# Kernel optimization log

Hardware: AMD Instinct MI355X
Metric: run time of the kernel (lower is better)

Reference implementation:

```python
import jax, jax.numpy as jnp
import numpy as np

DIM = 128
HEADS = 4
K = 7          # neighborhood kernel size
MLP_RATIO = 4
EPS = 1e-5


def setup_inputs() -> dict:
    key = jax.random.key(0)
    ks = jax.random.split(key, 8)
    B, H, W, C = 4, 64, 64, DIM
    hid = C * MLP_RATIO
    s = lambda k, shape: jax.random.normal(k, shape, jnp.float32) * 0.02
    return {
        "x": jax.random.normal(ks[0], (B, H, W, C), jnp.float32),
        "ln1_g": jnp.ones((C,), jnp.float32),
        "ln1_b": jnp.zeros((C,), jnp.float32),
        "qkv_w": s(ks[1], (C, 3 * C)),
        "qkv_b": jnp.zeros((3 * C,), jnp.float32),
        "rpb": s(ks[2], (HEADS, 2 * K - 1, 2 * K - 1)),
        "proj_w": s(ks[3], (C, C)),
        "proj_b": jnp.zeros((C,), jnp.float32),
        "ln2_g": jnp.ones((C,), jnp.float32),
        "ln2_b": jnp.zeros((C,), jnp.float32),
        "fc1_w": s(ks[4], (C, hid)),
        "fc1_b": jnp.zeros((hid,), jnp.float32),
        "fc2_w": s(ks[5], (hid, C)),
        "fc2_b": jnp.zeros((C,), jnp.float32),
    }


def _ln(x, g, b):
    m = jnp.mean(x, axis=-1, keepdims=True)
    v = jnp.mean(jnp.square(x - m), axis=-1, keepdims=True)
    return (x - m) * jax.lax.rsqrt(v + EPS) * g + b


def _neigh_idx(L, k):
    # NATTEN border-clamped neighborhood: start = clamp(i - k//2, 0, L-k)
    i = jnp.arange(L)
    start = jnp.clip(i - k // 2, 0, L - k)
    idx = start[:, None] + jnp.arange(k)[None, :]        # [L, k] key positions
    rel = idx - i[:, None] + (k - 1)                     # [L, k] rpb indices in [0, 2k-2]
    return idx, rel


def _neighborhood_attention(x, qkv_w, qkv_b, rpb, proj_w, proj_b):
    B, H, W, C = x.shape
    nh, hd = HEADS, C // HEADS
    scale = hd ** -0.5
    qkv = (x @ qkv_w + qkv_b).reshape(B, H, W, 3, nh, hd)
    qkv = qkv.transpose(3, 0, 4, 1, 2, 5)                # [3, B, nh, H, W, hd]
    q, k_, v = qkv[0] * scale, qkv[1], qkv[2]
    ih, rh = _neigh_idx(H, K)
    iw, rw = _neigh_idx(W, K)
    # gather 7x7 neighborhoods: [B, nh, H, K, W, K, hd]
    kg = k_[:, :, ih][:, :, :, :, iw]
    vg = v[:, :, ih][:, :, :, :, iw]
    attn = jnp.einsum('bnywc,bnykxjc->bnyxkj', q, kg)    # [B, nh, H, W, K, K]
    bias = rpb[:, rh][:, :, :, rw]                       # [nh, H, K, W, K]
    attn = attn + bias.transpose(0, 1, 3, 2, 4)[None]
    a = jax.nn.softmax(attn.reshape(B, nh, H, W, K * K), axis=-1)
    a = a.reshape(B, nh, H, W, K, K)
    out = jnp.einsum('bnyxkj,bnykxjc->bnyxc', a, vg)     # [B, nh, H, W, hd]
    out = out.transpose(0, 2, 3, 1, 4).reshape(B, H, W, C)
    return out @ proj_w + proj_b


def reference(x, ln1_g, ln1_b, qkv_w, qkv_b, rpb, proj_w, proj_b,
              ln2_g, ln2_b, fc1_w, fc1_b, fc2_w, fc2_b):
    h = x + _neighborhood_attention(_ln(x, ln1_g, ln1_b), qkv_w, qkv_b, rpb, proj_w, proj_b)
    y = _ln(h, ln2_g, ln2_b)
    y = jax.nn.gelu(y @ fc1_w + fc1_b, approximate=False) @ fc2_w + fc2_b
    return h + y
```

## Files before the change

kernel.cpp:

```cpp
#include <hip/hip_runtime.h>
#include <math.h>

#define TOKS 16384
#define CDIM 128
#define NH 4
#define HD 32
#define HID 512
#define QSCALE 0.17677669529663687f
#define LEPS 1e-5f

typedef const float* fp;
typedef const unsigned short* bfp16;
typedef __attribute__((ext_vector_type(8))) short bf16x8;
typedef __attribute__((ext_vector_type(4))) float f32x4;

__device__ inline unsigned int bfp2(float a, float b) {
    unsigned int ua = __float_as_uint(a); ua = (ua + 0x7FFFu + ((ua >> 16) & 1u)) >> 16;
    unsigned int ub = __float_as_uint(b); ub = (ub + 0x7FFFu + ((ub >> 16) & 1u)) >> 16;
    return ua | (ub << 16);
}
__device__ inline unsigned short bf1(float a) {
    unsigned int u = __float_as_uint(a);
    return (unsigned short)((u + 0x7FFFu + ((u >> 16) & 1u)) >> 16);
}
__device__ inline float lo16(unsigned int u) { return __uint_as_float(u << 16); }
__device__ inline float hi16(unsigned int u) { return __uint_as_float(u & 0xFFFF0000u); }

__global__ __launch_bounds__(256) void prep(fp qw, fp pw, fp f1w, fp f2w,
                                            fp x, fp g, fp b,
                                            unsigned short* __restrict__ wt,
                                            unsigned short* __restrict__ xn) {
    const int bid = blockIdx.x;
    if (bid < 768) {
        int e = bid * 256 + threadIdx.x;
        float v;
        if (e < 49152)       { int n = e >> 7,  k = e & 127;          v = qw[(size_t)k * 384 + n]; }
        else if (e < 65536)  { int i = e - 49152;  int n = i >> 7, k = i & 127; v = pw[(size_t)k * 128 + n]; }
        else if (e < 131072) { int i = e - 65536;  int n = i >> 7, k = i & 127; v = f1w[(size_t)k * 512 + n]; }
        else                 { int i = e - 131072; int n = i >> 9, k = i & 511; v = f2w[(size_t)k * 128 + n]; }
        wt[e] = bf1(v);
    } else {
        const int t = threadIdx.x;
        const int row = (bid - 768) * 8 + (t >> 5);
        const int l = t & 31;
        const float4 v = *(const float4*)(x + (size_t)row * CDIM + l * 4);
        float s = v.x + v.y + v.z + v.w;
        float q = v.x * v.x + v.y * v.y + v.z * v.z + v.w * v.w;
#pragma unroll
        for (int m = 16; m >= 1; m >>= 1) { s += __shfl_xor(s, m); q += __shfl_xor(q, m); }
        float mu = s * (1.f / 128.f);
        float rs = rsqrtf(q * (1.f / 128.f) - mu * mu + LEPS);
        const float4 gv = *(const float4*)(g + l * 4);
        const float4 bv = *(const float4*)(b + l * 4);
        float a0 = (v.x - mu) * rs * gv.x + bv.x, a1 = (v.y - mu) * rs * gv.y + bv.y;
        float a2 = (v.z - mu) * rs * gv.z + bv.z, a3 = (v.w - mu) * rs * gv.w + bv.w;
        uint2 o; o.x = bfp2(a0, a1); o.y = bfp2(a2, a3);
        *(uint2*)(xn + (size_t)row * CDIM + l * 4) = o;
    }
}


__global__ __launch_bounds__(256) void k1_mfma(bfp16 xn, bfp16 wt0, fp wb,
                                               float* __restrict__ qb,
                                               unsigned short* __restrict__ kvb) {
    __shared__ unsigned int lds[12288];
    const int m0 = blockIdx.x * 128;
    const int nb = blockIdx.y * 64;
    const int tid = threadIdx.x;
#pragma unroll
    for (int i = 0; i < 8; i++) {
        int slot = tid + i * 256;
        int m = slot >> 4, c16 = slot & 15;
        const uint4 v4 = *(const uint4*)(xn + (size_t)(m0 + m) * CDIM + c16 * 8);
        *(uint4*)&lds[m * 64 + (c16 ^ (m & 15)) * 4] = v4;
    }
#pragma unroll
    for (int i = 0; i < 4; i++) {
        int slot = tid + i * 256;
        int n = slot >> 4, c16 = slot & 15;
        const uint4 v4 = *(const uint4*)(wt0 + (size_t)(nb + n) * 128 + c16 * 8);
        *(uint4*)&lds[8192 + n * 64 + (c16 ^ (n & 15)) * 4] = v4;
    }
    __syncthreads();

    const int lane = tid & 63, wid = tid >> 6, quad = lane >> 4, l16 = lane & 15;
    f32x4 acc[2][4];
#pragma unroll
    for (int mt = 0; mt < 2; mt++)
#pragma unroll
        for (int nt = 0; nt < 4; nt++) acc[mt][nt] = (f32x4){0.f, 0.f, 0.f, 0.f};
#pragma unroll
    for (int kk = 0; kk < 4; kk++) {
        int c = kk * 4 + quad;
        bf16x8 a0 = *(bf16x8*)&lds[(wid * 32 + l16) * 64 + (c ^ l16) * 4];
        bf16x8 a1 = *(bf16x8*)&lds[(wid * 32 + 16 + l16) * 64 + (c ^ l16) * 4];
#pragma unroll
        for (int nt = 0; nt < 4; nt++) {
            bf16x8 bf = *(bf16x8*)&lds[8192 + (nt * 16 + l16) * 64 + (c ^ l16) * 4];
            acc[0][nt] = __builtin_amdgcn_mfma_f32_16x16x32_bf16(a0, bf, acc[0][nt], 0, 0, 0);
            acc[1][nt] = __builtin_amdgcn_mfma_f32_16x16x32_bf16(a1, bf, acc[1][nt], 0, 0, 0);
        }
    }
#pragma unroll
    for (int nt = 0; nt < 4; nt++) {
        int col = nb + nt * 16 + l16;
        float bias = wb[col];
#pragma unroll
        for (int mt = 0; mt < 2; mt++)
#pragma unroll
            for (int r = 0; r < 4; r++) {
                int row = m0 + wid * 32 + mt * 16 + quad * 4 + r;
                float vres = acc[mt][nt][r] + bias;
                if (col < 128)
                    qb[(size_t)row * 128 + col] = vres * QSCALE;
                else if (col < 256)
                    kvb[(size_t)row * 256 + (col - 128)] = bf1(vres);
                else
                    kvb[(size_t)row * 256 + 128 + (col - 256)] = bf1(vres);
            }
    }
}

__global__ __launch_bounds__(256) void k2_attn(const float* __restrict__ qb,
                                               const unsigned short* __restrict__ kvb,
                                               fp rpb, unsigned short* __restrict__ attnb) {
    const int gid = blockIdx.x * 256 + threadIdx.x;
    const int d = gid & 3;
    const int g = (gid >> 2) & 3;
    const int head = (gid >> 4) & 3;
    const int token = gid >> 6;
    const int bb = token >> 12;
    const int y = (token >> 6) & 63;
    const int xx = token & 63;
    const int sy = min(max(y - 3, 0), 57);
    const int sx = min(max(xx - 3, 0), 57);

    const int koff = head * HD + d * 8;
    float q[8];
    {
        const float4* qp = (const float4*)(qb + (size_t)token * 128 + koff);
        float4 q0 = qp[0], q1 = qp[1];
        q[0] = q0.x; q[1] = q0.y; q[2] = q0.z; q[3] = q0.w;
        q[4] = q1.x; q[5] = q1.y; q[6] = q1.z; q[7] = q1.w;
    }

    const float* rp = rpb + head * 169 + (sy - y + 6) * 13 + (sx - xx + 6);
    const int nbase = (bb << 12) + sy * 64 + sx;

    float sc[13];
#pragma unroll
    for (int i = 0; i < 13; i++) {
        int n = g * 13 + i;
        bool ok = n < 49;
        int nn = ok ? n : 48;
        int dy = nn / 7, dx = nn - dy * 7;
        const uint4 kk = *(const uint4*)(kvb + (size_t)(nbase + dy * 64 + dx) * 256 + koff);
        float s = q[0] * lo16(kk.x) + q[1] * hi16(kk.x)
                + q[2] * lo16(kk.y) + q[3] * hi16(kk.y)
                + q[4] * lo16(kk.z) + q[5] * hi16(kk.z)
                + q[6] * lo16(kk.w) + q[7] * hi16(kk.w);
        s += __shfl_xor(s, 1);
        s += __shfl_xor(s, 2);
        sc[i] = ok ? (s + rp[dy * 13 + dx]) : -1e30f;
    }
    float mx = sc[0];
#pragma unroll
    for (int l = 1; l < 13; l++) mx = fmaxf(mx, sc[l]);
    mx = fmaxf(mx, __shfl_xor(mx, 4));
    mx = fmaxf(mx, __shfl_xor(mx, 8));
    float sum = 0.f;
#pragma unroll
    for (int l = 0; l < 13; l++) { sc[l] = __expf(sc[l] - mx); sum += sc[l]; }
    sum += __shfl_xor(sum, 4);
    sum += __shfl_xor(sum, 8);
    float inv = 1.f / sum;

    float o[8];
#pragma unroll
    for (int i = 0; i < 8; i++) o[i] = 0.f;
#pragma unroll
    for (int i = 0; i < 13; i++) {
        int n = g * 13 + i;
        int nn = (n < 49) ? n : 48;
        int dy = nn / 7, dx = nn - dy * 7;
        float p = sc[i] * inv;
        const uint4 vv = *(const uint4*)(kvb + (size_t)(nbase + dy * 64 + dx) * 256 + 128 + koff);
        o[0] += p * lo16(vv.x); o[1] += p * hi16(vv.x);
        o[2] += p * lo16(vv.y); o[3] += p * hi16(vv.y);
        o[4] += p * lo16(vv.z); o[5] += p * hi16(vv.z);
        o[6] += p * lo16(vv.w); o[7] += p * hi16(vv.w);
    }
#pragma unroll
    for (int i = 0; i < 8; i++) {
        o[i] += __shfl_xor(o[i], 4);
        o[i] += __shfl_xor(o[i], 8);
    }
    if (g == 0) {
        uint4 ov;
        ov.x = bfp2(o[0], o[1]); ov.y = bfp2(o[2], o[3]);
        ov.z = bfp2(o[4], o[5]); ov.w = bfp2(o[6], o[7]);
        *(uint4*)(attnb + (size_t)token * 128 + koff) = ov;
    }
}

__global__ __launch_bounds__(256) void k3_mfma(bfp16 attnb, fp x, bfp16 wt1, fp pb,
                                               fp g2, fp b2,
                                               float* __restrict__ h,
                                               unsigned short* __restrict__ hn) {
    __shared__ unsigned int lds[12288];
    const int m0 = blockIdx.x * 64;
    const int tid = threadIdx.x;
#pragma unroll
    for (int i = 0; i < 4; i++) {
        int slot = tid + i * 256;
        int m = slot >> 4, c16 = slot & 15;
        const uint4 v4 = *(const uint4*)(attnb + (size_t)(m0 + m) * CDIM + c16 * 8);
        *(uint4*)&lds[m * 64 + (c16 ^ (m & 15)) * 4] = v4;
    }
#pragma unroll
    for (int i = 0; i < 8; i++) {
        int slot = tid + i * 256;
        int n = slot >> 4, c16 = slot & 15;
        const uint4 v4 = *(const uint4*)(wt1 + (size_t)n * 128 + c16 * 8);
        *(uint4*)&lds[4096 + n * 64 + (c16 ^ (n & 15)) * 4] = v4;
    }
    __syncthreads();

    const int lane = tid & 63, wid = tid >> 6, quad = lane >> 4, l16 = lane & 15;
    const int mrow = wid * 16 + l16;
    f32x4 acc[8];
#pragma unroll
    for (int nt = 0; nt < 8; nt++) acc[nt] = (f32x4){0.f, 0.f, 0.f, 0.f};
#pragma unroll
    for (int kk = 0; kk < 4; kk++) {
        int c = kk * 4 + quad;
        bf16x8 a = *(bf16x8*)&lds[mrow * 64 + (c ^ l16) * 4];
#pragma unroll
        for (int nt = 0; nt < 8; nt++) {
            bf16x8 bf = *(bf16x8*)&lds[4096 + (nt * 16 + l16) * 64 + (c ^ l16) * 4];
            acc[nt] = __builtin_amdgcn_mfma_f32_16x16x32_bf16(a, bf, acc[nt], 0, 0, 0);
        }
    }
    float s[4] = {0.f, 0.f, 0.f, 0.f}, q[4] = {0.f, 0.f, 0.f, 0.f};
#pragma unroll
    for (int nt = 0; nt < 8; nt++) {
        int col = nt * 16 + l16;
        float bias = pb[col];
#pragma unroll
        for (int r = 0; r < 4; r++) {
            int row = m0 + wid * 16 + quad * 4 + r;
            float hv = x[(size_t)row * CDIM + col] + acc[nt][r] + bias;
            h[(size_t)row * CDIM + col] = hv;
            acc[nt][r] = hv;
            s[r] += hv; q[r] += hv * hv;
        }
    }
#pragma unroll
    for (int m = 1; m <= 8; m <<= 1) {
#pragma unroll
        for (int r = 0; r < 4; r++) {
            s[r] += __shfl_xor(s[r], m);
            q[r] += __shfl_xor(q[r], m);
        }
    }
    float mu[4], rs[4];
#pragma unroll
    for (int r = 0; r < 4; r++) {
        mu[r] = s[r] * (1.f / 128.f);
        rs[r] = rsqrtf(q[r] * (1.f / 128.f) - mu[r] * mu[r] + LEPS);
    }
#pragma unroll
    for (int nt = 0; nt < 8; nt++) {
        int col = nt * 16 + l16;
        float gg = g2[col], bb = b2[col];
#pragma unroll
        for (int r = 0; r < 4; r++) {
            int row = m0 + wid * 16 + quad * 4 + r;
            hn[(size_t)row * CDIM + col] = bf1((acc[nt][r] - mu[r]) * rs[r] * gg + bb);
        }
    }
}

__global__ __launch_bounds__(256) void k4_mfma(bfp16 hn, bfp16 wt2, fp wb,
                                               unsigned short* __restrict__ y1) {
    __shared__ unsigned int lds[12288];
    const int m0 = blockIdx.x * 128;
    const int nb = blockIdx.y * 64;
    const int tid = threadIdx.x;
#pragma unroll
    for (int i = 0; i < 8; i++) {
        int slot = tid + i * 256;
        int m = slot >> 4, c16 = slot & 15;
        const uint4 v4 = *(const uint4*)(hn + (size_t)(m0 + m) * CDIM + c16 * 8);
        *(uint4*)&lds[m * 64 + (c16 ^ (m & 15)) * 4] = v4;
    }
#pragma unroll
    for (int i = 0; i < 4; i++) {
        int slot = tid + i * 256;
        int n = slot >> 4, c16 = slot & 15;
        const uint4 v4 = *(const uint4*)(wt2 + (size_t)(nb + n) * 128 + c16 * 8);
        *(uint4*)&lds[8192 + n * 64 + (c16 ^ (n & 15)) * 4] = v4;
    }
    __syncthreads();

    const int lane = tid & 63, wid = tid >> 6, quad = lane >> 4, l16 = lane & 15;
    f32x4 acc[2][4];
#pragma unroll
    for (int mt = 0; mt < 2; mt++)
#pragma unroll
        for (int nt = 0; nt < 4; nt++) acc[mt][nt] = (f32x4){0.f, 0.f, 0.f, 0.f};
#pragma unroll
    for (int kk = 0; kk < 4; kk++) {
        int c = kk * 4 + quad;
        bf16x8 a0 = *(bf16x8*)&lds[(wid * 32 + l16) * 64 + (c ^ l16) * 4];
        bf16x8 a1 = *(bf16x8*)&lds[(wid * 32 + 16 + l16) * 64 + (c ^ l16) * 4];
#pragma unroll
        for (int nt = 0; nt < 4; nt++) {
            bf16x8 bf = *(bf16x8*)&lds[8192 + (nt * 16 + l16) * 64 + (c ^ l16) * 4];
            acc[0][nt] = __builtin_amdgcn_mfma_f32_16x16x32_bf16(a0, bf, acc[0][nt], 0, 0, 0);
            acc[1][nt] = __builtin_amdgcn_mfma_f32_16x16x32_bf16(a1, bf, acc[1][nt], 0, 0, 0);
        }
    }
#pragma unroll
    for (int nt = 0; nt < 4; nt++) {
        int col = nb + nt * 16 + l16;
        float bias = wb[col];
#pragma unroll
        for (int mt = 0; mt < 2; mt++)
#pragma unroll
            for (int r = 0; r < 4; r++) {
                int row = m0 + wid * 32 + mt * 16 + quad * 4 + r;
                float z = acc[mt][nt][r] + bias;
                y1[(size_t)row * HID + col] = bf1(0.5f * z * (1.f + erff(z * 0.70710678118654752f)));
            }
    }
}

__global__ __launch_bounds__(256) void k5_mfma(bfp16 y1, fp h, bfp16 wt3, fp wb,
                                               float* __restrict__ out) {
    __shared__ unsigned int lds[12288];
    const int m0 = blockIdx.x * 128;
    const int nb = blockIdx.y * 64;
    const int tid = threadIdx.x;
    const int lane = tid & 63, wid = tid >> 6, quad = lane >> 4, l16 = lane & 15;
    f32x4 acc[2][4];
#pragma unroll
    for (int mt = 0; mt < 2; mt++)
#pragma unroll
        for (int nt = 0; nt < 4; nt++) acc[mt][nt] = (f32x4){0.f, 0.f, 0.f, 0.f};

    for (int kc = 0; kc < 4; kc++) {
        if (kc) __syncthreads();
#pragma unroll
        for (int i = 0; i < 8; i++) {
            int slot = tid + i * 256;
            int m = slot >> 4, c16 = slot & 15;
            const uint4 v4 = *(const uint4*)(y1 + (size_t)(m0 + m) * HID + kc * 128 + c16 * 8);
            *(uint4*)&lds[m * 64 + (c16 ^ (m & 15)) * 4] = v4;
        }
#pragma unroll
        for (int i = 0; i < 4; i++) {
            int slot = tid + i * 256;
            int n = slot >> 4, c16 = slot & 15;
            const uint4 v4 = *(const uint4*)(wt3 + (size_t)(nb + n) * 512 + kc * 128 + c16 * 8);
            *(uint4*)&lds[8192 + n * 64 + (c16 ^ (n & 15)) * 4] = v4;
        }
        __syncthreads();
#pragma unroll
        for (int kk = 0; kk < 4; kk++) {
            int c = kk * 4 + quad;
            bf16x8 a0 = *(bf16x8*)&lds[(wid * 32 + l16) * 64 + (c ^ l16) * 4];
            bf16x8 a1 = *(bf16x8*)&lds[(wid * 32 + 16 + l16) * 64 + (c ^ l16) * 4];
#pragma unroll
            for (int nt = 0; nt < 4; nt++) {
                bf16x8 bf = *(bf16x8*)&lds[8192 + (nt * 16 + l16) * 64 + (c ^ l16) * 4];
                acc[0][nt] = __builtin_amdgcn_mfma_f32_16x16x32_bf16(a0, bf, acc[0][nt], 0, 0, 0);
                acc[1][nt] = __builtin_amdgcn_mfma_f32_16x16x32_bf16(a1, bf, acc[1][nt], 0, 0, 0);
            }
        }
    }
#pragma unroll
    for (int nt = 0; nt < 4; nt++) {
        int col = nb + nt * 16 + l16;
        float bias = wb[col];
#pragma unroll
        for (int mt = 0; mt < 2; mt++)
#pragma unroll
            for (int r = 0; r < 4; r++) {
                int row = m0 + wid * 32 + mt * 16 + quad * 4 + r;
                out[(size_t)row * CDIM + col] = h[(size_t)row * CDIM + col] + acc[mt][nt][r] + bias;
            }
    }
}

extern "C" void kernel_launch(void* const* d_in, const int* in_sizes, int n_in,
                              void* d_out, int out_size, void* d_ws, size_t ws_size,
                              hipStream_t stream) {
    fp x      = (fp)d_in[0];
    fp ln1_g  = (fp)d_in[1];
    fp ln1_b  = (fp)d_in[2];
    fp qkv_w  = (fp)d_in[3];
    fp qkv_b  = (fp)d_in[4];
    fp rpb    = (fp)d_in[5];
    fp proj_w = (fp)d_in[6];
    fp proj_b = (fp)d_in[7];
    fp ln2_g  = (fp)d_in[8];
    fp ln2_b  = (fp)d_in[9];
    fp fc1_w  = (fp)d_in[10];
    fp fc1_b  = (fp)d_in[11];
    fp fc2_w  = (fp)d_in[12];
    fp fc2_b  = (fp)d_in[13];
    float* out = (float*)d_out;

    float* ws = (float*)d_ws;
    float* h  = ws;
    unsigned short* xn = (unsigned short*)(h + (size_t)TOKS * CDIM);
    unsigned short* hn = xn + (size_t)TOKS * CDIM;
    float* qb = (float*)(hn + (size_t)TOKS * CDIM);
    unsigned short* kvb   = (unsigned short*)(qb + (size_t)TOKS * CDIM);
    unsigned short* attnb = kvb + (size_t)TOKS * 256;
    unsigned short* wt    = attnb + (size_t)TOKS * CDIM;
    unsigned short* y1    = (unsigned short*)qb;

    unsigned short* wt0 = wt;
    unsigned short* wt1 = wt + 49152;
    unsigned short* wt2 = wt + 65536;
    unsigned short* wt3 = wt + 131072;

    prep<<<768 + TOKS / 8, 256, 0, stream>>>(qkv_w, proj_w, fc1_w, fc2_w, x, ln1_g, ln1_b, wt, xn);
    k1_mfma<<<dim3(TOKS / 128, 6), 256, 0, stream>>>(xn, wt0, qkv_b, qb, kvb);
    k2_attn<<<TOKS * NH * 16 / 256, 256, 0, stream>>>(qb, kvb, rpb, attnb);
    k3_mfma<<<TOKS / 64, 256, 0, stream>>>(attnb, x, wt1, proj_b, ln2_g, ln2_b, h, hn);
    k4_mfma<<<dim3(TOKS / 128, 8), 256, 0, stream>>>(hn, wt2, fc1_b, y1);
    k5_mfma<<<dim3(TOKS / 128, 2), 256, 0, stream>>>(y1, h, wt3, fc2_b, out);
}
```

Before: 149.3 us.

## Stage K/V neighborhood halo in LDS for 2x2 query tiles in attention kernel

```diff
diff --git a/kernel.cpp b/kernel.cpp
--- a/kernel.cpp
+++ b/kernel.cpp
@@ -124,28 +124,42 @@
 __global__ __launch_bounds__(256) void k2_attn(const float* __restrict__ qb,
                                                const unsigned short* __restrict__ kvb,
                                                fp rpb, unsigned short* __restrict__ attnb) {
-    const int gid = blockIdx.x * 256 + threadIdx.x;
-    const int d = gid & 3;
-    const int g = (gid >> 2) & 3;
-    const int head = (gid >> 4) & 3;
-    const int token = gid >> 6;
-    const int bb = token >> 12;
-    const int y = (token >> 6) & 63;
-    const int xx = token & 63;
-    const int sy = min(max(y - 3, 0), 57);
-    const int sx = min(max(xx - 3, 0), 57);
-
-    const int koff = head * HD + d * 8;
+    __shared__ unsigned int ldsu[64 * 68];
+    const int tile = blockIdx.x;
+    const int bb = blockIdx.y;
+    const int ty0 = (tile >> 5) * 2, tx0 = (tile & 31) * 2;
+    const int ky0 = min(max(ty0 - 3, 0), 56);
+    const int kx0 = min(max(tx0 - 3, 0), 56);
+    const int tid = threadIdx.x;
+
+#pragma unroll
+    for (int i = 0; i < 4; i++) {
+        int slot = tid + i * 256;
+        int p = slot >> 4, c16 = slot & 15;
+        int gr = (bb << 12) + (ky0 + (p >> 3)) * 64 + kx0 + (p & 7);
+        const uint4 v4 = *(const uint4*)(kvb + (size_t)gr * 256 + c16 * 8);
+        *(uint4*)&ldsu[p * 68 + c16 * 4] = v4;
+    }
+
+    const int u = tid >> 4;
+    const int tl = u >> 2, head = u & 3;
+    const int lane16 = tid & 15;
+    const int d = lane16 & 3, g = lane16 >> 2;
+    const int qy = ty0 + (tl >> 1), qx = tx0 + (tl & 1);
+    const int token = (bb << 12) + qy * 64 + qx;
+
     float q[8];
     {
-        const float4* qp = (const float4*)(qb + (size_t)token * 128 + koff);
+        const float4* qp = (const float4*)(qb + (size_t)token * 128 + head * HD + d * 8);
         float4 q0 = qp[0], q1 = qp[1];
         q[0] = q0.x; q[1] = q0.y; q[2] = q0.z; q[3] = q0.w;
         q[4] = q1.x; q[5] = q1.y; q[6] = q1.z; q[7] = q1.w;
     }
-
-    const float* rp = rpb + head * 169 + (sy - y + 6) * 13 + (sx - xx + 6);
-    const int nbase = (bb << 12) + sy * 64 + sx;
+    const int gsy = min(max(qy - 3, 0), 57), gsx = min(max(qx - 3, 0), 57);
+    const int ly = gsy - ky0, lx = gsx - kx0;
+    const float* rp = rpb + head * 169 + (gsy - qy + 6) * 13 + (gsx - qx + 6);
+    const int dwoff = head * 16 + d * 4;
+    __syncthreads();
 
     float sc[13];
 #pragma unroll
@@ -154,7 +168,8 @@
         bool ok = n < 49;
         int nn = ok ? n : 48;
         int dy = nn / 7, dx = nn - dy * 7;
-        const uint4 kk = *(const uint4*)(kvb + (size_t)(nbase + dy * 64 + dx) * 256 + koff);
+        int p = (ly + dy) * 8 + (lx + dx);
+        const uint4 kk = *(const uint4*)&ldsu[p * 68 + dwoff];
         float s = q[0] * lo16(kk.x) + q[1] * hi16(kk.x)
                 + q[2] * lo16(kk.y) + q[3] * hi16(kk.y)
                 + q[4] * lo16(kk.z) + q[5] * hi16(kk.z)
@@ -163,6 +178,16 @@
         s += __shfl_xor(s, 2);
         sc[i] = ok ? (s + rp[dy * 13 + dx]) : -1e30f;
     }
+    __syncthreads();
+
+#pragma unroll
+    for (int i = 0; i < 4; i++) {
+        int slot = tid + i * 256;
+        int p = slot >> 4, c16 = slot & 15;
+        int gr = (bb << 12) + (ky0 + (p >> 3)) * 64 + kx0 + (p & 7);
+        const uint4 v4 = *(const uint4*)(kvb + (size_t)gr * 256 + 128 + c16 * 8);
+        *(uint4*)&ldsu[p * 68 + c16 * 4] = v4;
+    }
     float mx = sc[0];
 #pragma unroll
     for (int l = 1; l < 13; l++) mx = fmaxf(mx, sc[l]);
@@ -174,6 +199,7 @@
     sum += __shfl_xor(sum, 4);
     sum += __shfl_xor(sum, 8);
     float inv = 1.f / sum;
+    __syncthreads();
 
     float o[8];
 #pragma unroll
@@ -183,12 +209,13 @@
         int n = g * 13 + i;
         int nn = (n < 49) ? n : 48;
         int dy = nn / 7, dx = nn - dy * 7;
-        float p = sc[i] * inv;
-        const uint4 vv = *(const uint4*)(kvb + (size_t)(nbase + dy * 64 + dx) * 256 + 128 + koff);
-        o[0] += p * lo16(vv.x); o[1] += p * hi16(vv.x);
-        o[2] += p * lo16(vv.y); o[3] += p * hi16(vv.y);
-        o[4] += p * lo16(vv.z); o[5] += p * hi16(vv.z);
-        o[6] += p * lo16(vv.w); o[7] += p * hi16(vv.w);
+        int p = (ly + dy) * 8 + (lx + dx);
+        float pr = sc[i] * inv;
+        const uint4 vv = *(const uint4*)&ldsu[p * 68 + dwoff];
+        o[0] += pr * lo16(vv.x); o[1] += pr * hi16(vv.x);
+        o[2] += pr * lo16(vv.y); o[3] += pr * hi16(vv.y);
+        o[4] += pr * lo16(vv.z); o[5] += pr * hi16(vv.z);
+        o[6] += pr * lo16(vv.w); o[7] += pr * hi16(vv.w);
     }
 #pragma unroll
     for (int i = 0; i < 8; i++) {
@@ -199,7 +226,7 @@
         uint4 ov;
         ov.x = bfp2(o[0], o[1]); ov.y = bfp2(o[2], o[3]);
         ov.z = bfp2(o[4], o[5]); ov.w = bfp2(o[6], o[7]);
-        *(uint4*)(attnb + (size_t)token * 128 + koff) = ov;
+        *(uint4*)(attnb + (size_t)token * 128 + head * HD + d * 8) = ov;
     }
 }
 
@@ -429,7 +456,7 @@
 
     prep<<<768 + TOKS / 8, 256, 0, stream>>>(qkv_w, proj_w, fc1_w, fc2_w, x, ln1_g, ln1_b, wt, xn);
     k1_mfma<<<dim3(TOKS / 128, 6), 256, 0, stream>>>(xn, wt0, qkv_b, qb, kvb);
-    k2_attn<<<TOKS * NH * 16 / 256, 256, 0, stream>>>(qb, kvb, rpb, attnb);
+    k2_attn<<<dim3(1024, 4), 256, 0, stream>>>(qb, kvb, rpb, attnb);
     k3_mfma<<<TOKS / 64, 256, 0, stream>>>(attnb, x, wt1, proj_b, ln2_g, ln2_b, h, hn);
     k4_mfma<<<dim3(TOKS / 128, 8), 256, 0, stream>>>(hn, wt2, fc1_b, y1);
     k5_mfma<<<dim3(TOKS / 128, 2), 256, 0, stream>>>(y1, h, wt3, fc2_b, out);
```

New measurement: 150.2 us. Within noise of the previous version (+0.6%).

## Store Q in bf16 in a fused QKV buffer and remap blocks per XCD

Applied to the files above, without the earlier changes.

```diff
diff --git a/kernel.cpp b/kernel.cpp
--- a/kernel.cpp
+++ b/kernel.cpp
@@ -61,11 +61,12 @@
 
 
 __global__ __launch_bounds__(256) void k1_mfma(bfp16 xn, bfp16 wt0, fp wb,
-                                               float* __restrict__ qb,
-                                               unsigned short* __restrict__ kvb) {
+                                               unsigned short* __restrict__ qkvb) {
     __shared__ unsigned int lds[12288];
-    const int m0 = blockIdx.x * 128;
-    const int nb = blockIdx.y * 64;
+    const int bid = blockIdx.x;
+    const int xcd = bid & 7, idx = bid >> 3;
+    const int m0 = (xcd * 16 + (idx & 15)) * 128;
+    const int nb = (idx >> 4) * 64;
     const int tid = threadIdx.x;
 #pragma unroll
     for (int i = 0; i < 8; i++) {
@@ -105,30 +106,26 @@
     for (int nt = 0; nt < 4; nt++) {
         int col = nb + nt * 16 + l16;
         float bias = wb[col];
+        float sc = (col < 128) ? QSCALE : 1.f;
 #pragma unroll
         for (int mt = 0; mt < 2; mt++)
 #pragma unroll
             for (int r = 0; r < 4; r++) {
                 int row = m0 + wid * 32 + mt * 16 + quad * 4 + r;
-                float vres = acc[mt][nt][r] + bias;
-                if (col < 128)
-                    qb[(size_t)row * 128 + col] = vres * QSCALE;
-                else if (col < 256)
-                    kvb[(size_t)row * 256 + (col - 128)] = bf1(vres);
-                else
-                    kvb[(size_t)row * 256 + 128 + (col - 256)] = bf1(vres);
+                qkvb[(size_t)row * 384 + col] = bf1((acc[mt][nt][r] + bias) * sc);
             }
     }
 }
 
-__global__ __launch_bounds__(256) void k2_attn(const float* __restrict__ qb,
-                                               const unsigned short* __restrict__ kvb,
-                                               fp rpb, unsigned short* __restrict__ attnb) {
-    const int gid = blockIdx.x * 256 + threadIdx.x;
-    const int d = gid & 3;
-    const int g = (gid >> 2) & 3;
-    const int head = (gid >> 4) & 3;
-    const int token = gid >> 6;
+__global__ __launch_bounds__(256) void k2_attn(bfp16 qkvb, fp rpb,
+                                               unsigned short* __restrict__ attnb) {
+    const int bid = blockIdx.x;
+    const int xcd = bid & 7, idx = bid >> 3;
+    const int token = xcd * 2048 + idx * 4 + (threadIdx.x >> 6);
+    const int lane = threadIdx.x & 63;
+    const int d = lane & 3;
+    const int g = (lane >> 2) & 3;
+    const int head = lane >> 4;
     const int bb = token >> 12;
     const int y = (token >> 6) & 63;
     const int xx = token & 63;
@@ -138,10 +135,9 @@
     const int koff = head * HD + d * 8;
     float q[8];
     {
-        const float4* qp = (const float4*)(qb + (size_t)token * 128 + koff);
-        float4 q0 = qp[0], q1 = qp[1];
-        q[0] = q0.x; q[1] = q0.y; q[2] = q0.z; q[3] = q0.w;
-        q[4] = q1.x; q[5] = q1.y; q[6] = q1.z; q[7] = q1.w;
+        const uint4 qv = *(const uint4*)(qkvb + (size_t)token * 384 + koff);
+        q[0] = lo16(qv.x); q[1] = hi16(qv.x); q[2] = lo16(qv.y); q[3] = hi16(qv.y);
+        q[4] = lo16(qv.z); q[5] = hi16(qv.z); q[6] = lo16(qv.w); q[7] = hi16(qv.w);
     }
 
     const float* rp = rpb + head * 169 + (sy - y + 6) * 13 + (sx - xx + 6);
@@ -154,7 +150,7 @@
         bool ok = n < 49;
         int nn = ok ? n : 48;
         int dy = nn / 7, dx = nn - dy * 7;
-        const uint4 kk = *(const uint4*)(kvb + (size_t)(nbase + dy * 64 + dx) * 256 + koff);
+        const uint4 kk = *(const uint4*)(qkvb + (size_t)(nbase + dy * 64 + dx) * 384 + 128 + koff);
         float s = q[0] * lo16(kk.x) + q[1] * hi16(kk.x)
                 + q[2] * lo16(kk.y) + q[3] * hi16(kk.y)
                 + q[4] * lo16(kk.z) + q[5] * hi16(kk.z)
@@ -184,7 +180,7 @@
         int nn = (n < 49) ? n : 48;
         int dy = nn / 7, dx = nn - dy * 7;
         float p = sc[i] * inv;
-        const uint4 vv = *(const uint4*)(kvb + (size_t)(nbase + dy * 64 + dx) * 256 + 128 + koff);
+        const uint4 vv = *(const uint4*)(qkvb + (size_t)(nbase + dy * 64 + dx) * 384 + 256 + koff);
         o[0] += p * lo16(vv.x); o[1] += p * hi16(vv.x);
         o[2] += p * lo16(vv.y); o[3] += p * hi16(vv.y);
         o[4] += p * lo16(vv.z); o[5] += p * hi16(vv.z);
@@ -284,8 +280,10 @@
 __global__ __launch_bounds__(256) void k4_mfma(bfp16 hn, bfp16 wt2, fp wb,
                                                unsigned short* __restrict__ y1) {
     __shared__ unsigned int lds[12288];
-    const int m0 = blockIdx.x * 128;
-    const int nb = blockIdx.y * 64;
+    const int bid = blockIdx.x;
+    const int xcd = bid & 7, idx = bid >> 3;
+    const int m0 = (xcd * 16 + (idx & 15)) * 128;
+    const int nb = (idx >> 4) * 64;
     const int tid = threadIdx.x;
 #pragma unroll
     for (int i = 0; i < 8; i++) {
@@ -339,8 +337,10 @@
 __global__ __launch_bounds__(256) void k5_mfma(bfp16 y1, fp h, bfp16 wt3, fp wb,
                                                float* __restrict__ out) {
     __shared__ unsigned int lds[12288];
-    const int m0 = blockIdx.x * 128;
-    const int nb = blockIdx.y * 64;
+    const int bid = blockIdx.x;
+    const int xcd = bid & 7, idx = bid >> 3;
+    const int m0 = (xcd * 16 + (idx & 15)) * 128;
+    const int nb = (idx >> 4) * 64;
     const int tid = threadIdx.x;
     const int lane = tid & 63, wid = tid >> 6, quad = lane >> 4, l16 = lane & 15;
     f32x4 acc[2][4];
@@ -412,15 +412,13 @@
     fp fc2_b  = (fp)d_in[13];
     float* out = (float*)d_out;
 
-    float* ws = (float*)d_ws;
-    float* h  = ws;
-    unsigned short* xn = (unsigned short*)(h + (size_t)TOKS * CDIM);
-    unsigned short* hn = xn + (size_t)TOKS * CDIM;
-    float* qb = (float*)(hn + (size_t)TOKS * CDIM);
-    unsigned short* kvb   = (unsigned short*)(qb + (size_t)TOKS * CDIM);
-    unsigned short* attnb = kvb + (size_t)TOKS * 256;
-    unsigned short* wt    = attnb + (size_t)TOKS * CDIM;
-    unsigned short* y1    = (unsigned short*)qb;
+    unsigned short* qkvb  = (unsigned short*)d_ws;
+    unsigned short* attnb = qkvb + (size_t)TOKS * 384;
+    unsigned short* y1    = qkvb;
+    unsigned short* xn    = qkvb + (size_t)TOKS * 512;
+    unsigned short* hn    = xn + (size_t)TOKS * CDIM;
+    unsigned short* wt    = hn + (size_t)TOKS * CDIM;
+    float* h = (float*)(wt + 196608);
 
     unsigned short* wt0 = wt;
     unsigned short* wt1 = wt + 49152;
@@ -428,9 +426,9 @@
     unsigned short* wt3 = wt + 131072;
 
     prep<<<768 + TOKS / 8, 256, 0, stream>>>(qkv_w, proj_w, fc1_w, fc2_w, x, ln1_g, ln1_b, wt, xn);
-    k1_mfma<<<dim3(TOKS / 128, 6), 256, 0, stream>>>(xn, wt0, qkv_b, qb, kvb);
-    k2_attn<<<TOKS * NH * 16 / 256, 256, 0, stream>>>(qb, kvb, rpb, attnb);
+    k1_mfma<<<768, 256, 0, stream>>>(xn, wt0, qkv_b, qkvb);
+    k2_attn<<<4096, 256, 0, stream>>>(qkvb, rpb, attnb);
     k3_mfma<<<TOKS / 64, 256, 0, stream>>>(attnb, x, wt1, proj_b, ln2_g, ln2_b, h, hn);
-    k4_mfma<<<dim3(TOKS / 128, 8), 256, 0, stream>>>(hn, wt2, fc1_b, y1);
-    k5_mfma<<<dim3(TOKS / 128, 2), 256, 0, stream>>>(y1, h, wt3, fc2_b, out);
-}
+    k4_mfma<<<1024, 256, 0, stream>>>(hn, wt2, fc1_b, y1);
+    k5_mfma<<<256, 256, 0, stream>>>(y1, h, wt3, fc2_b, out);
+}
```

Measured after the change: 155.8 us. 4.4% more time.
